# Kernel tuning notes

Hardware: AMD Instinct MI355X
Metric: run time of the kernel (lower is better)

Reference implementation:

```python
import jax, jax.numpy as jnp
import numpy as np


def dense_image_warp(img, flow):
    """Faithful port of tfa.image.dense_image_warp(img, flow):
    output[b,i,j] = bilinear_sample(img[b], (i - flow[b,i,j,0], j - flow[b,i,j,1]))
    with floors clamped to [0, size-2] and alphas clipped to [0,1] (TFA semantics).
    """
    B, H, W, C = img.shape
    gy = jnp.arange(H, dtype=flow.dtype)[None, :, None]   # [1,H,1]
    gx = jnp.arange(W, dtype=flow.dtype)[None, None, :]   # [1,1,W]
    # query = grid - flow
    qy = gy - flow[..., 0]                                 # [B,H,W]
    qx = gx - flow[..., 1]
    fy = jnp.clip(jnp.floor(qy), 0.0, H - 2)
    fx = jnp.clip(jnp.floor(qx), 0.0, W - 2)
    ay = jnp.clip(qy - fy, 0.0, 1.0)[..., None]            # [B,H,W,1]
    ax = jnp.clip(qx - fx, 0.0, 1.0)[..., None]
    fy_i = fy.astype(jnp.int32)
    fx_i = fx.astype(jnp.int32)

    flat = img.reshape(B, H * W, C)

    def gather(yy, xx):  # yy,xx: [B,H,W] int32
        idx = (yy * W + xx).reshape(B, H * W, 1)
        return jnp.take_along_axis(flat, idx, axis=1).reshape(B, H, W, C)

    tl = gather(fy_i,     fx_i)
    tr = gather(fy_i,     fx_i + 1)
    bl = gather(fy_i + 1, fx_i)
    br = gather(fy_i + 1, fx_i + 1)

    top = tl + (tr - tl) * ax
    bot = bl + (br - bl) * ax
    return top + (bot - top) * ay


def setup_inputs() -> dict:
    key = jax.random.key(0)
    k1, k2 = jax.random.split(key)
    img = jax.random.normal(k1, (16, 256, 512, 32), dtype=jnp.float32)
    flow = jax.random.normal(k2, (16, 256, 512, 2), dtype=jnp.float32)
    return {"img": img, "flow": flow}


def reference(img, flow):
    # InvWarpFlow.call: dense_image_warp(img, -flow)
    return dense_image_warp(img, -flow)
```

## Files before the change

kernel.cpp:

```cpp
#include <hip/hip_runtime.h>


typedef float floatx4 __attribute__((ext_vector_type(4)));

__global__ __launch_bounds__(256, 1) void InvWarpFlow_kernel(
    const float* __restrict__ img,
    const float* __restrict__ flow,
    float* __restrict__ out)
{
    constexpr int H = 256, W = 512, C = 32;
    constexpr int TW = 8, TH = 16;
    constexpr int TILES_X = W / TW;
    constexpr int TILES_Y = H / TH;
    constexpr int NBLK = 16 * TILES_X * TILES_Y;
    constexpr int PER_XCD = NBLK / 8;

    int bid = blockIdx.x;
    int logical = (bid & 7) * PER_XCD + (bid >> 3);

    int tx = logical & (TILES_X - 1);
    int r  = logical >> 6;
    int ty = r & (TILES_Y - 1);
    int b  = r >> 4;

    int t  = threadIdx.x;
    int cg = t & 7;
    int s  = t >> 3;
    int lx = s & 7;
    int wv = s >> 3;

    int x  = tx * TW + lx;
    int y0 = ty * TH + wv * 4;
    int pix0 = ((b << 8) + y0) * W + x;

    float2 f[4];
    #pragma unroll
    for (int k = 0; k < 4; ++k)
        f[k] = *reinterpret_cast<const float2*>(flow + (size_t)(pix0 + k * W) * 2);

    const float* ib = img + (size_t)b * H * W * C + cg * 4;
    const float* baseT[4];
    const float* baseB[4];
    float ax[4], ay[4];
    #pragma unroll
    for (int k = 0; k < 4; ++k) {
        float qy = (float)(y0 + k) + f[k].x;
        float qx = (float)x + f[k].y;
        float fy = fminf(fmaxf(floorf(qy), 0.0f), (float)(H - 2));
        float fx = fminf(fmaxf(floorf(qx), 0.0f), (float)(W - 2));
        ay[k] = fminf(fmaxf(qy - fy, 0.0f), 1.0f);
        ax[k] = fminf(fmaxf(qx - fx, 0.0f), 1.0f);
        baseT[k] = ib + ((size_t)(int)fy * W + (int)fx) * C;
        baseB[k] = baseT[k] + (size_t)W * C;
    }

    floatx4 tl[4], tr[4], bl[4], br[4];
    #pragma unroll
    for (int k = 0; k < 4; ++k) {
        asm volatile("global_load_dwordx4 %0, %2, off\n\t"
                     "global_load_dwordx4 %1, %2, off offset:128"
                     : "=&v"(tl[k]), "=&v"(tr[k]) : "v"(baseT[k]));
        asm volatile("global_load_dwordx4 %0, %2, off\n\t"
                     "global_load_dwordx4 %1, %2, off offset:128"
                     : "=&v"(bl[k]), "=&v"(br[k]) : "v"(baseB[k]));
    }

    asm volatile("s_waitcnt vmcnt(0)"
                 : "+v"(tl[0]), "+v"(tl[1]), "+v"(tl[2]), "+v"(tl[3]),
                   "+v"(tr[0]), "+v"(tr[1]), "+v"(tr[2]), "+v"(tr[3]),
                   "+v"(bl[0]), "+v"(bl[1]), "+v"(bl[2]), "+v"(bl[3]),
                   "+v"(br[0]), "+v"(br[1]), "+v"(br[2]), "+v"(br[3])
                 :: "memory");
    __builtin_amdgcn_sched_barrier(0);

    #pragma unroll
    for (int k = 0; k < 4; ++k) {
        floatx4 top = tl[k] + (tr[k] - tl[k]) * ax[k];
        floatx4 bot = bl[k] + (br[k] - bl[k]) * ax[k];
        floatx4 o   = top + (bot - top) * ay[k];
        __builtin_nontemporal_store(
            o, reinterpret_cast<floatx4*>(out + (size_t)(pix0 + k * W) * C + cg * 4));
    }
}

extern "C" void kernel_launch(void* const* d_in, const int* in_sizes, int n_in,
                              void* d_out, int out_size, void* d_ws, size_t ws_size,
                              hipStream_t stream) {
    const float* img  = (const float*)d_in[0];
    const float* flow = (const float*)d_in[1];
    float* out = (float*)d_out;

    constexpr int NBLK = 16384;
    InvWarpFlow_kernel<<<NBLK, 256, 0, stream>>>(img, flow, out);
}
```

Before: 99.58 us.

## Process eight rows per thread with split waitcnt to overlap loads and stores

Measured after the change: 99.22 us. Within noise of the previous version (-0.4%).

```diff
diff --git a/kernel.cpp b/kernel.cpp
--- a/kernel.cpp
+++ b/kernel.cpp
@@ -2,6 +2,7 @@
 
 
 typedef float floatx4 __attribute__((ext_vector_type(4)));
+typedef float floatx2 __attribute__((ext_vector_type(2)));
 
 __global__ __launch_bounds__(256, 1) void InvWarpFlow_kernel(
     const float* __restrict__ img,
@@ -9,68 +10,65 @@
     float* __restrict__ out)
 {
     constexpr int H = 256, W = 512, C = 32;
-    constexpr int TW = 8, TH = 16;
+    constexpr int TW = 32;
+    constexpr int RPT = 8;
     constexpr int TILES_X = W / TW;
-    constexpr int TILES_Y = H / TH;
-    constexpr int NBLK = 16 * TILES_X * TILES_Y;
+    constexpr int YSTR = H / RPT;
+    constexpr int NBLK = 16 * TILES_X * YSTR;
     constexpr int PER_XCD = NBLK / 8;
 
     int bid = blockIdx.x;
     int logical = (bid & 7) * PER_XCD + (bid >> 3);
-
     int tx = logical & (TILES_X - 1);
-    int r  = logical >> 6;
-    int ty = r & (TILES_Y - 1);
-    int b  = r >> 4;
+    int r  = logical >> 4;
+    int ys = r & (YSTR - 1);
+    int b  = r >> 5;
 
     int t  = threadIdx.x;
     int cg = t & 7;
-    int s  = t >> 3;
-    int lx = s & 7;
-    int wv = s >> 3;
+    int sl = t >> 3;
+    int x  = tx * TW + sl;
+    int y0 = ys * RPT;
 
-    int x  = tx * TW + lx;
-    int y0 = ty * TH + wv * 4;
-    int pix0 = ((b << 8) + y0) * W + x;
+    const float* ibase = img  + (size_t)(b << 8) * W * C + cg * 4;
+    const float* fbase = flow + ((size_t)((b << 8) + y0) * W + x) * 2;
+    float*       obase = out  + ((size_t)((b << 8) + y0) * W + x) * C + cg * 4;
 
-    float2 f[4];
+    floatx2 f[RPT];
     #pragma unroll
-    for (int k = 0; k < 4; ++k)
-        f[k] = *reinterpret_cast<const float2*>(flow + (size_t)(pix0 + k * W) * 2);
+    for (int k = 0; k < RPT; ++k)
+        f[k] = *reinterpret_cast<const floatx2*>(fbase + (size_t)k * (W * 2));
 
-    const float* ib = img + (size_t)b * H * W * C + cg * 4;
-    const float* baseT[4];
-    const float* baseB[4];
-    float ax[4], ay[4];
+    const float* bT[RPT];
+    float ax[RPT], ay[RPT];
     #pragma unroll
-    for (int k = 0; k < 4; ++k) {
+    for (int k = 0; k < RPT; ++k) {
         float qy = (float)(y0 + k) + f[k].x;
         float qx = (float)x + f[k].y;
         float fy = fminf(fmaxf(floorf(qy), 0.0f), (float)(H - 2));
         float fx = fminf(fmaxf(floorf(qx), 0.0f), (float)(W - 2));
         ay[k] = fminf(fmaxf(qy - fy, 0.0f), 1.0f);
         ax[k] = fminf(fmaxf(qx - fx, 0.0f), 1.0f);
-        baseT[k] = ib + ((size_t)(int)fy * W + (int)fx) * C;
-        baseB[k] = baseT[k] + (size_t)W * C;
+        bT[k] = ibase + ((size_t)(int)fy * W + (int)fx) * C;
     }
 
-    floatx4 tl[4], tr[4], bl[4], br[4];
+    floatx4 tl[RPT], tr[RPT], bl[RPT], br[RPT];
     #pragma unroll
-    for (int k = 0; k < 4; ++k) {
+    for (int k = 0; k < RPT; ++k) {
+        const float* bB = bT[k] + (size_t)W * C;
         asm volatile("global_load_dwordx4 %0, %2, off\n\t"
                      "global_load_dwordx4 %1, %2, off offset:128"
-                     : "=&v"(tl[k]), "=&v"(tr[k]) : "v"(baseT[k]));
+                     : "=&v"(tl[k]), "=&v"(tr[k]) : "v"(bT[k]));
         asm volatile("global_load_dwordx4 %0, %2, off\n\t"
                      "global_load_dwordx4 %1, %2, off offset:128"
-                     : "=&v"(bl[k]), "=&v"(br[k]) : "v"(baseB[k]));
+                     : "=&v"(bl[k]), "=&v"(br[k]) : "v"(bB));
     }
 
-    asm volatile("s_waitcnt vmcnt(0)"
-                 : "+v"(tl[0]), "+v"(tl[1]), "+v"(tl[2]), "+v"(tl[3]),
-                   "+v"(tr[0]), "+v"(tr[1]), "+v"(tr[2]), "+v"(tr[3]),
-                   "+v"(bl[0]), "+v"(bl[1]), "+v"(bl[2]), "+v"(bl[3]),
-                   "+v"(br[0]), "+v"(br[1]), "+v"(br[2]), "+v"(br[3])
-                 :: "memory");
+    asm volatile("s_waitcnt vmcnt(16)"
+        : "+v"(tl[0]), "+v"(tl[1]), "+v"(tl[2]), "+v"(tl[3]),
+          "+v"(tr[0]), "+v"(tr[1]), "+v"(tr[2]), "+v"(tr[3]),
+          "+v"(bl[0]), "+v"(bl[1]), "+v"(bl[2]), "+v"(bl[3]),
+          "+v"(br[0]), "+v"(br[1]), "+v"(br[2]), "+v"(br[3]) :: "memory");
     __builtin_amdgcn_sched_barrier(0);
 
     #pragma unroll
@@ -79,7 +77,23 @@
         floatx4 bot = bl[k] + (br[k] - bl[k]) * ax[k];
         floatx4 o   = top + (bot - top) * ay[k];
         __builtin_nontemporal_store(
-            o, reinterpret_cast<floatx4*>(out + (size_t)(pix0 + k * W) * C + cg * 4));
+            o, reinterpret_cast<floatx4*>(obase + (size_t)k * (W * C)));
+    }
+
+    asm volatile("s_waitcnt vmcnt(4)"
+        : "+v"(tl[4]), "+v"(tl[5]), "+v"(tl[6]), "+v"(tl[7]),
+          "+v"(tr[4]), "+v"(tr[5]), "+v"(tr[6]), "+v"(tr[7]),
+          "+v"(bl[4]), "+v"(bl[5]), "+v"(bl[6]), "+v"(bl[7]),
+          "+v"(br[4]), "+v"(br[5]), "+v"(br[6]), "+v"(br[7]) :: "memory");
+    __builtin_amdgcn_sched_barrier(0);
+
+    #pragma unroll
+    for (int k = 4; k < 8; ++k) {
+        floatx4 top = tl[k] + (tr[k] - tl[k]) * ax[k];
+        floatx4 bot = bl[k] + (br[k] - bl[k]) * ax[k];
+        floatx4 o   = top + (bot - top) * ay[k];
+        __builtin_nontemporal_store(
+            o, reinterpret_cast<floatx4*>(obase + (size_t)k * (W * C)));
     }
 }
 
@@ -90,6 +104,6 @@
     const float* flow = (const float*)d_in[1];
     float* out = (float*)d_out;
 
-    constexpr int NBLK = 16384;
+    constexpr int NBLK = 8192;
     InvWarpFlow_kernel<<<NBLK, 256, 0, stream>>>(img, flow, out);
 }
```
